# Performance work log

Hardware: AMD Instinct MI355X
Metric: run time of the kernel (lower is better)

The kernel has to match this reference:

```python
import jax, jax.numpy as jnp
import numpy as np

B, S, D, H = 2, 2048, 1024, 16
DK = D // H

def setup_inputs() -> dict:
    key = jax.random.key(0)
    ks = jax.random.split(key, 8)
    inp = {
        "Q": jax.random.normal(ks[0], (B, S, D), dtype=jnp.float32),
        "K": jax.random.normal(ks[1], (B, S, D), dtype=jnp.float32),
        "V": jax.random.normal(ks[2], (B, S, D), dtype=jnp.float32),
        "mask": jax.random.randint(ks[3], (B, 1, S, S), 0, 2, dtype=jnp.int32),
        # nn.Linear weights, shape [out_features, in_features], no bias
        "Wq": jax.random.normal(ks[4], (D, D), dtype=jnp.float32) / np.sqrt(D),
        "Wk": jax.random.normal(ks[5], (D, D), dtype=jnp.float32) / np.sqrt(D),
        "Wv": jax.random.normal(ks[6], (D, D), dtype=jnp.float32) / np.sqrt(D),
        "Wo": jax.random.normal(ks[7], (D, D), dtype=jnp.float32) / np.sqrt(D),
    }
    return inp

def reference(Q, K, V, mask, Wq, Wk, Wv, Wo):
    b, s, d = Q.shape
    # projections: y = x @ W.T (torch nn.Linear convention)
    q = (Q @ Wq.T).reshape(b, s, H, DK).transpose(0, 2, 1, 3)  # [b,h,s,dk]
    k = (K @ Wk.T).reshape(b, -1, H, DK).transpose(0, 2, 1, 3)
    v = (V @ Wv.T).reshape(b, -1, H, DK).transpose(0, 2, 1, 3)
    score = jnp.einsum("bhqd,bhkd->bhqk", q, k) / jnp.sqrt(jnp.float32(DK))
    # faithful to source: masked positions get value 1e-9 BEFORE softmax
    score = jnp.where(mask == 0, jnp.float32(1e-9), score)
    attn = jax.nn.softmax(score, axis=-1)
    # dropout p=0.1 treated as eval-mode identity
    out = jnp.einsum("bhqk,bhkd->bhqd", attn, v)  # [b,h,s,dk]
    out = out.transpose(0, 2, 1, 3).reshape(b, s, d)
    return out @ Wo.T
```

## Files before the change

### kernel.cpp

```cpp
#include <hip/hip_runtime.h>

typedef unsigned short u16;
typedef unsigned char  u8;
typedef unsigned long long u64;
typedef __attribute__((ext_vector_type(8))) short bf16x8;
typedef __attribute__((ext_vector_type(4))) float f32x4;

constexpr int B_  = 2;
constexpr int S_  = 2048;
constexpr int D_  = 1024;
constexpr int H_  = 16;
constexpr int DK_ = 64;
constexpr int NROW = B_ * S_;
constexpr size_t QSZ  = (size_t)B_ * H_ * S_ * DK_;
constexpr size_t XBSZ = (size_t)NROW * D_;
constexpr size_t WBSZ = (size_t)D_ * D_;
constexpr size_t MSZ  = (size_t)B_ * S_ * S_;
constexpr size_t MPKB = MSZ / 8;

__device__ __forceinline__ u16 f2bf(float f) {
    union { float f; unsigned u; } c; c.f = f;
    unsigned r = c.u + 0x7fffu + ((c.u >> 16) & 1u);
    return (u16)(r >> 16);
}
__device__ __forceinline__ unsigned pack2(float a, float b) {
    return (unsigned)f2bf(a) | ((unsigned)f2bf(b) << 16);
}
__device__ __forceinline__ unsigned cvt_pk_bf16(float a, float b) {
    unsigned r;
    asm("v_cvt_pk_bf16_f32 %0, %1, %2" : "=v"(r) : "v"(a), "v"(b));
    return r;
}

__device__ __forceinline__ void gl_lds16(const u16* g, u16* l) {
    __builtin_amdgcn_global_load_lds(
        (const __attribute__((address_space(1))) void*)g,
        (__attribute__((address_space(3))) void*)l, 16, 0, 0);
}

__global__ __launch_bounds__(256)
void cvt7m(const float* __restrict__ s0, const float* __restrict__ s1,
           const float* __restrict__ s2, const float* __restrict__ s3,
           const float* __restrict__ s4, const float* __restrict__ s5,
           const float* __restrict__ s6, const int* __restrict__ mk,
           u16* __restrict__ d0, u16* __restrict__ d1, u16* __restrict__ d2,
           u16* __restrict__ d3, u16* __restrict__ d4, u16* __restrict__ d5,
           u16* __restrict__ d6, u8* __restrict__ mp)
{
    constexpr size_t XT = 3 * XBSZ;
    constexpr int NCF = (int)((3 * XBSZ + 4 * WBSZ) / 2048);
    constexpr int NCM = (int)(MSZ / 2048);

    for (int c = blockIdx.x; c < NCF + NCM; c += gridDim.x) {
        if (c < NCF) {
            const size_t base = (size_t)c * 2048;
            const float* s; u16* d; size_t off;
            if (base < XT) {
                const int a = (int)(base >> 22);
                off = base & (XBSZ - 1);
                s = (a == 0) ? s0 : (a == 1) ? s1 : s2;
                d = (a == 0) ? d0 : (a == 1) ? d1 : d2;
            } else {
                const size_t r = base - XT;
                const int a = (int)(r >> 20);
                off = r & (WBSZ - 1);
                s = (a == 0) ? s3 : (a == 1) ? s4 : (a == 2) ? s5 : s6;
                d = (a == 0) ? d3 : (a == 1) ? d4 : (a == 2) ? d5 : d6;
            }
            const size_t e = off + (size_t)threadIdx.x * 8;
            const float4 x0 = *(const float4*)(s + e);
            const float4 x1 = *(const float4*)(s + e + 4);
            uint4 p;
            p.x = pack2(x0.x, x0.y); p.y = pack2(x0.z, x0.w);
            p.z = pack2(x1.x, x1.y); p.w = pack2(x1.z, x1.w);
            *(uint4*)(d + e) = p;
        } else {
            const size_t e = (size_t)(c - NCF) * 2048 + (size_t)threadIdx.x * 8;
            const int4 x0 = *(const int4*)(mk + e);
            const int4 x1 = *(const int4*)(mk + e + 4);
            unsigned bv = (unsigned)(x0.x != 0)        | ((unsigned)(x0.y != 0) << 1)
                        | ((unsigned)(x0.z != 0) << 2) | ((unsigned)(x0.w != 0) << 3)
                        | ((unsigned)(x1.x != 0) << 4) | ((unsigned)(x1.y != 0) << 5)
                        | ((unsigned)(x1.z != 0) << 6) | ((unsigned)(x1.w != 0) << 7);
            mp[e >> 3] = (u8)bv;
        }
    }
}

__global__ __launch_bounds__(256, 3)
void qkv_gemm(const u16* __restrict__ Xq, const u16* __restrict__ Xk,
              const u16* __restrict__ Xv,
              const u16* __restrict__ Wq, const u16* __restrict__ Wk,
              const u16* __restrict__ Wv,
              u16* __restrict__ Yq, u16* __restrict__ Yk, u16* __restrict__ Yv)
{
    __shared__ u16 As[128 * 32];
    __shared__ u16 Bs[128 * 32];

    const int z = blockIdx.z;
    const u16* X = (z == 0) ? Xq : (z == 1) ? Xk : Xv;
    const u16* W = (z == 0) ? Wq : (z == 1) ? Wk : Wv;
    u16*       Y = (z == 0) ? Yq : (z == 1) ? Yk : Yv;
    const float osc = (z == 0) ? 0.125f : 1.0f;

    const int tid  = threadIdx.x;
    const int lane = tid & 63;
    const int w    = tid >> 6;
    const int quad = lane >> 4;
    const int lq   = lane & 15;
    const int wm   = (w & 1) << 6;
    const int wn   = (w >> 1) << 6;

    const int m0 = blockIdx.x << 7;
    const int n0 = blockIdx.y << 7;

    const int srow = tid >> 2;
    const int scol = (tid & 3) << 3;
    const u16* ga0 = X + (size_t)(m0 + srow) * D_ + scol;
    const u16* ga1 = ga0 + (size_t)64 * D_;
    const u16* gb0 = W + (size_t)(n0 + srow) * D_ + scol;
    const u16* gb1 = gb0 + (size_t)64 * D_;

    u16* la0 = As + (size_t)w * 512;
    u16* la1 = As + 2048 + (size_t)w * 512;
    u16* lb0 = Bs + (size_t)w * 512;
    u16* lb1 = Bs + 2048 + (size_t)w * 512;

    f32x4 acc[4][4];
#pragma unroll
    for (int i = 0; i < 4; ++i)
#pragma unroll
        for (int j = 0; j < 4; ++j) acc[i][j] = (f32x4){0.f, 0.f, 0.f, 0.f};

    for (int kt = 0; kt < D_; kt += 32) {
        __syncthreads();
        gl_lds16(ga0 + kt, la0);
        gl_lds16(ga1 + kt, la1);
        gl_lds16(gb0 + kt, lb0);
        gl_lds16(gb1 + kt, lb1);
        __syncthreads();

        bf16x8 af[4], bf[4];
#pragma unroll
        for (int t = 0; t < 4; ++t) {
            af[t] = *(const bf16x8*)&As[(size_t)(wm + (t << 4) + lq) * 32 + (quad << 3)];
            bf[t] = *(const bf16x8*)&Bs[(size_t)(wn + (t << 4) + lq) * 32 + (quad << 3)];
        }
#pragma unroll
        for (int i = 0; i < 4; ++i)
#pragma unroll
            for (int j = 0; j < 4; ++j)
                acc[i][j] = __builtin_amdgcn_mfma_f32_16x16x32_bf16(
                    af[i], bf[j], acc[i][j], 0, 0, 0);
    }

#pragma unroll
    for (int i = 0; i < 4; ++i)
#pragma unroll
        for (int j = 0; j < 4; ++j)
#pragma unroll
            for (int r = 0; r < 4; ++r) {
                const int grow = m0 + wm + (i << 4) + (quad << 2) + r;
                const int of   = n0 + wn + (j << 4) + lq;
                const int b = grow >> 11, s = grow & (S_ - 1);
                const int h = of >> 6,    dk = of & 63;
                Y[(((size_t)(b * H_ + h)) * S_ + s) * DK_ + dk] =
                    f2bf(acc[i][j][r] * osc);
            }
}

__global__ __launch_bounds__(256, 3)
void out_gemm(const u16* __restrict__ X, const u16* __restrict__ W,
              float* __restrict__ Y)
{
    __shared__ u16 As[128 * 32];
    __shared__ u16 Bs[128 * 32];

    const int tid  = threadIdx.x;
    const int lane = tid & 63;
    const int w    = tid >> 6;
    const int quad = lane >> 4;
    const int lq   = lane & 15;
    const int wm   = (w & 1) << 6;
    const int wn   = (w >> 1) << 6;

    const int m0 = blockIdx.x << 7;
    const int n0 = blockIdx.y << 7;

    const int srow = tid >> 2;
    const int scol = (tid & 3) << 3;
    const u16* ga0 = X + (size_t)(m0 + srow) * D_ + scol;
    const u16* ga1 = ga0 + (size_t)64 * D_;
    const u16* gb0 = W + (size_t)(n0 + srow) * D_ + scol;
    const u16* gb1 = gb0 + (size_t)64 * D_;

    u16* la0 = As + (size_t)w * 512;
    u16* la1 = As + 2048 + (size_t)w * 512;
    u16* lb0 = Bs + (size_t)w * 512;
    u16* lb1 = Bs + 2048 + (size_t)w * 512;

    f32x4 acc[4][4];
#pragma unroll
    for (int i = 0; i < 4; ++i)
#pragma unroll
        for (int j = 0; j < 4; ++j) acc[i][j] = (f32x4){0.f, 0.f, 0.f, 0.f};

    for (int kt = 0; kt < D_; kt += 32) {
        __syncthreads();
        gl_lds16(ga0 + kt, la0);
        gl_lds16(ga1 + kt, la1);
        gl_lds16(gb0 + kt, lb0);
        gl_lds16(gb1 + kt, lb1);
        __syncthreads();

        bf16x8 af[4], bf[4];
#pragma unroll
        for (int t = 0; t < 4; ++t) {
            af[t] = *(const bf16x8*)&As[(size_t)(wm + (t << 4) + lq) * 32 + (quad << 3)];
            bf[t] = *(const bf16x8*)&Bs[(size_t)(wn + (t << 4) + lq) * 32 + (quad << 3)];
        }
#pragma unroll
        for (int i = 0; i < 4; ++i)
#pragma unroll
            for (int j = 0; j < 4; ++j)
                acc[i][j] = __builtin_amdgcn_mfma_f32_16x16x32_bf16(
                    af[i], bf[j], acc[i][j], 0, 0, 0);
    }

#pragma unroll
    for (int i = 0; i < 4; ++i)
#pragma unroll
        for (int j = 0; j < 4; ++j)
#pragma unroll
            for (int r = 0; r < 4; ++r) {
                const int grow = m0 + wm + (i << 4) + (quad << 2) + r;
                const int gcol = n0 + wn + (j << 4) + lq;
                Y[(size_t)grow * D_ + gcol] = acc[i][j][r];
            }
}

constexpr int AP = 72;

__global__ __launch_bounds__(256, 2)
void attn_mfma5(const u16* __restrict__ qb, const u16* __restrict__ kb,
                const u16* __restrict__ vb, const u8* __restrict__ mpk,
                u16* __restrict__ ctx)
{
    __shared__ u16 Qs[128][AP];
    __shared__ u16 Ks[64][AP];
    __shared__ u16 Vt[64][AP];
    __shared__ u16 Ps[128][AP];

    const int tid  = threadIdx.x;
    const int lane = tid & 63;
    const int w    = tid >> 6;
    const int quad = lane >> 4;
    const int lq   = lane & 15;
    const int w32  = w << 5;

    const int q0 = blockIdx.x << 7;
    const int h  = blockIdx.y;
    const int b  = blockIdx.z;

    const u16* qbh = qb + (((size_t)b * H_ + h) * S_ + q0) * DK_;
    const u16* kbh = kb + ((size_t)b * H_ + h) * S_ * DK_;
    const u16* vbh = vb + ((size_t)b * H_ + h) * S_ * DK_;
    const u8*  mbh = mpk + (size_t)b * S_ * (S_ / 8);

    {
        const int r = tid >> 1, c = (tid & 1) << 5;
#pragma unroll
        for (int u = 0; u < 4; ++u)
            *(uint4*)&Qs[r][c + (u << 3)] =
                *(const uint4*)&qbh[(size_t)r * DK_ + c + (u << 3)];
    }
    __syncthreads();
    bf16x8 aQ[2][2];
#pragma unroll
    for (int i = 0; i < 2; ++i) {
        aQ[i][0] = *(const bf16x8*)&Qs[w32 + (i << 4) + lq][quad << 3];
        aQ[i][1] = *(const bf16x8*)&Qs[w32 + (i << 4) + lq][32 + (quad << 3)];
    }

    f32x4 O[2][4];
    float lsum[2][4];
#pragma unroll
    for (int i = 0; i < 2; ++i)
#pragma unroll
        for (int t = 0; t < 4; ++t) O[i][t] = (f32x4){0.f, 0.f, 0.f, 0.f};
#pragma unroll
    for (int i = 0; i < 2; ++i)
#pragma unroll
        for (int r = 0; r < 4; ++r) lsum[i][r] = 0.f;

    const int ksr = tid >> 2, ksc = (tid & 3) << 4;
    const int vkey = lane, vsc = w << 4;
    const int vpc  = ((vkey & 15) << 2) | (vkey >> 4);

    uint4 kr0, kr1; ushort4 vr[4];
    {
        kr0 = *(const uint4*)&kbh[(size_t)ksr * DK_ + ksc];
        kr1 = *(const uint4*)&kbh[(size_t)ksr * DK_ + ksc + 8];
#pragma unroll
        for (int u = 0; u < 4; ++u)
            vr[u] = *(const ushort4*)&vbh[(size_t)vkey * DK_ + vsc + (u << 2)];
    }

    const int qrow0 = q0 + w32 + (quad << 2);
    const u8* mrow = mbh + (size_t)qrow0 * (S_ / 8);

    for (int k0 = 0; k0 < S_; k0 += 64) {
        u64 mw[2][4];
#pragma unroll
        for (int i = 0; i < 2; ++i)
#pragma unroll
            for (int r = 0; r < 4; ++r)
                mw[i][r] = *(const u64*)&mrow[(size_t)((i << 4) + r) * (S_ / 8) + (k0 >> 3)];

        __syncthreads();
        {
            *(uint4*)&Ks[ksr][ksc]     = kr0;
            *(uint4*)&Ks[ksr][ksc + 8] = kr1;
            const u16 vv[16] = {
                vr[0].x, vr[0].y, vr[0].z, vr[0].w,
                vr[1].x, vr[1].y, vr[1].z, vr[1].w,
                vr[2].x, vr[2].y, vr[2].z, vr[2].w,
                vr[3].x, vr[3].y, vr[3].z, vr[3].w };
#pragma unroll
            for (int i = 0; i < 16; ++i)
                Vt[vsc + i][vpc] = vv[i];
        }
        __syncthreads();

        if (k0 + 64 < S_) {
            const size_t kb0 = (size_t)(k0 + 64 + ksr) * DK_ + ksc;
            kr0 = *(const uint4*)&kbh[kb0];
            kr1 = *(const uint4*)&kbh[kb0 + 8];
            const size_t vb0 = (size_t)(k0 + 64 + vkey) * DK_ + vsc;
#pragma unroll
            for (int u = 0; u < 4; ++u)
                vr[u] = *(const ushort4*)&vbh[vb0 + (u << 2)];
        }

        f32x4 st[2][4];
#pragma unroll
        for (int t = 0; t < 4; ++t) {
            const bf16x8 b0 = *(const bf16x8*)&Ks[(t << 4) + lq][quad << 3];
            const bf16x8 b1 = *(const bf16x8*)&Ks[(t << 4) + lq][32 + (quad << 3)];
#pragma unroll
            for (int i = 0; i < 2; ++i) {
                f32x4 c = {0.f, 0.f, 0.f, 0.f};
                c = __builtin_amdgcn_mfma_f32_16x16x32_bf16(aQ[i][0], b0, c, 0, 0, 0);
                c = __builtin_amdgcn_mfma_f32_16x16x32_bf16(aQ[i][1], b1, c, 0, 0, 0);
                st[i][t] = c;
            }
        }

#pragma unroll
        for (int i = 0; i < 2; ++i)
#pragma unroll
            for (int r = 0; r < 4; ++r) {
                const unsigned lo = (unsigned)mw[i][r];
                const unsigned hi = (unsigned)(mw[i][r] >> 32);
                float p0 = __expf(st[i][0][r]);
                float p1 = __expf(st[i][1][r]);
                float p2 = __expf(st[i][2][r]);
                float p3 = __expf(st[i][3][r]);
                p0 = ((lo >> lq) & 1u) ? p0 : 1.0f;
                p1 = ((lo >> (lq + 16)) & 1u) ? p1 : 1.0f;
                p2 = ((hi >> lq) & 1u) ? p2 : 1.0f;
                p3 = ((hi >> (lq + 16)) & 1u) ? p3 : 1.0f;
                lsum[i][r] += (p0 + p1) + (p2 + p3);
                uint2 pw;
                pw.x = cvt_pk_bf16(p0, p1);
                pw.y = cvt_pk_bf16(p2, p3);
                *(uint2*)&Ps[w32 + (i << 4) + (quad << 2) + r][lq << 2] = pw;
            }

        bf16x8 aP[2][2];
#pragma unroll
        for (int i = 0; i < 2; ++i) {
            aP[i][0] = *(const bf16x8*)&Ps[w32 + (i << 4) + lq][quad << 3];
            aP[i][1] = *(const bf16x8*)&Ps[w32 + (i << 4) + lq][32 + (quad << 3)];
        }
#pragma unroll
        for (int t = 0; t < 4; ++t) {
            const bf16x8 b0 = *(const bf16x8*)&Vt[(t << 4) + lq][quad << 3];
            const bf16x8 b1 = *(const bf16x8*)&Vt[(t << 4) + lq][32 + (quad << 3)];
#pragma unroll
            for (int i = 0; i < 2; ++i) {
                O[i][t] = __builtin_amdgcn_mfma_f32_16x16x32_bf16(aP[i][0], b0, O[i][t], 0, 0, 0);
                O[i][t] = __builtin_amdgcn_mfma_f32_16x16x32_bf16(aP[i][1], b1, O[i][t], 0, 0, 0);
            }
        }
    }

#pragma unroll
    for (int i = 0; i < 2; ++i)
#pragma unroll
        for (int r = 0; r < 4; ++r) {
#pragma unroll
            for (int off = 1; off < 16; off <<= 1)
                lsum[i][r] += __shfl_xor(lsum[i][r], off);
            lsum[i][r] = 1.0f / lsum[i][r];
        }

#pragma unroll
    for (int i = 0; i < 2; ++i)
#pragma unroll
        for (int t = 0; t < 4; ++t)
#pragma unroll
            for (int r = 0; r < 4; ++r) {
                const int row = qrow0 + (i << 4) + r;
                ctx[((size_t)b * S_ + row) * D_ + (h << 6) + (t << 4) + lq] =
                    f2bf(O[i][t][r] * lsum[i][r]);
            }
}

extern "C" void kernel_launch(void* const* d_in, const int* in_sizes, int n_in,
                              void* d_out, int out_size, void* d_ws, size_t ws_size,
                              hipStream_t stream)
{
    const float* Q    = (const float*)d_in[0];
    const float* K    = (const float*)d_in[1];
    const float* V    = (const float*)d_in[2];
    const int*   mask = (const int*)d_in[3];
    const float* Wq   = (const float*)d_in[4];
    const float* Wk   = (const float*)d_in[5];
    const float* Wv   = (const float*)d_in[6];
    const float* Wo   = (const float*)d_in[7];
    float* out = (float*)d_out;

    u16* xqb = (u16*)d_ws;
    u16* xkb = xqb + XBSZ;
    u16* xvb = xqb + 2 * XBSZ;
    u16* wqb = xqb + 3 * XBSZ;
    u16* wkb = wqb + WBSZ;
    u16* wvb = wqb + 2 * WBSZ;
    u16* wob = wqb + 3 * WBSZ;
    u16* qw  = wqb + 4 * WBSZ;
    u16* kw  = qw + QSZ;
    u16* vw  = qw + 2 * QSZ;
    u8*  mpk = (u8*)(qw + 3 * QSZ);
    u16* cx  = xqb;

    const dim3 blk(256);

    hipLaunchKernelGGL(cvt7m, dim3(2048), blk, 0, stream,
                       Q, K, V, Wq, Wk, Wv, Wo, mask,
                       xqb, xkb, xvb, wqb, wkb, wvb, wob, mpk);
    hipLaunchKernelGGL(qkv_gemm, dim3(NROW / 128, D_ / 128, 3), blk, 0, stream,
                       xqb, xkb, xvb, wqb, wkb, wvb, qw, kw, vw);
    hipLaunchKernelGGL(attn_mfma5, dim3(S_ / 128, H_, B_), blk, 0, stream,
                       qw, kw, vw, mpk, cx);
    hipLaunchKernelGGL(out_gemm, dim3(NROW / 128, D_ / 128), blk, 0, stream,
                       cx, wob, out);
}
```

Before: 254.8 us.

## Split attention key range across two warp groups and merge partial results

```diff
diff --git a/kernel.cpp b/kernel.cpp
--- a/kernel.cpp
+++ b/kernel.cpp
@@ -222,7 +222,7 @@
 #pragma unroll
         for (int i = 0; i < 4; ++i)
 #pragma unroll
-            for (int j = 0; j < 4; ++j)
+            for (int j = 0; j < 2 * 2; ++j)
                 acc[i][j] = __builtin_amdgcn_mfma_f32_16x16x32_bf16(
                     af[i], bf[j], acc[i][j], 0, 0, 0);
     }
@@ -241,45 +241,39 @@
 
 constexpr int AP = 72;
 
-__global__ __launch_bounds__(256, 2)
-void attn_mfma5(const u16* __restrict__ qb, const u16* __restrict__ kb,
+__global__ __launch_bounds__(512, 4)
+void attn_mfma6(const u16* __restrict__ qb, const u16* __restrict__ kb,
                 const u16* __restrict__ vb, const u8* __restrict__ mpk,
                 u16* __restrict__ ctx)
 {
-    __shared__ u16 Qs[128][AP];
-    __shared__ u16 Ks[64][AP];
-    __shared__ u16 Vt[64][AP];
-    __shared__ u16 Ps[128][AP];
+    __shared__ __align__(16) u16 Ks[2][64][AP];
+    __shared__ __align__(16) u16 Vt[2][64][AP];
+    __shared__ __align__(16) u16 Ps[2][128][AP];
 
     const int tid  = threadIdx.x;
     const int lane = tid & 63;
     const int w    = tid >> 6;
+    const int g    = w >> 2;
+    const int wl   = w & 3;
     const int quad = lane >> 4;
     const int lq   = lane & 15;
-    const int w32  = w << 5;
+    const int w32  = wl << 5;
+    const int tg   = tid & 255;
 
     const int q0 = blockIdx.x << 7;
     const int h  = blockIdx.y;
     const int b  = blockIdx.z;
 
     const u16* qbh = qb + (((size_t)b * H_ + h) * S_ + q0) * DK_;
-    const u16* kbh = kb + ((size_t)b * H_ + h) * S_ * DK_;
-    const u16* vbh = vb + ((size_t)b * H_ + h) * S_ * DK_;
-    const u8*  mbh = mpk + (size_t)b * S_ * (S_ / 8);
-
-    {
-        const int r = tid >> 1, c = (tid & 1) << 5;
-#pragma unroll
-        for (int u = 0; u < 4; ++u)
-            *(uint4*)&Qs[r][c + (u << 3)] =
-                *(const uint4*)&qbh[(size_t)r * DK_ + c + (u << 3)];
-    }
-    __syncthreads();
+    const u16* kbh = kb + ((size_t)b * H_ + h) * S_ * DK_ + ((size_t)(g << 10)) * DK_;
+    const u16* vbh = vb + ((size_t)b * H_ + h) * S_ * DK_ + ((size_t)(g << 10)) * DK_;
+
     bf16x8 aQ[2][2];
 #pragma unroll
     for (int i = 0; i < 2; ++i) {
-        aQ[i][0] = *(const bf16x8*)&Qs[w32 + (i << 4) + lq][quad << 3];
-        aQ[i][1] = *(const bf16x8*)&Qs[w32 + (i << 4) + lq][32 + (quad << 3)];
+        const size_t qr = (size_t)(w32 + (i << 4) + lq) * DK_;
+        aQ[i][0] = *(const bf16x8*)&qbh[qr + (quad << 3)];
+        aQ[i][1] = *(const bf16x8*)&qbh[qr + 32 + (quad << 3)];
     }
 
     f32x4 O[2][4];
@@ -293,8 +287,8 @@
 #pragma unroll
         for (int r = 0; r < 4; ++r) lsum[i][r] = 0.f;
 
-    const int ksr = tid >> 2, ksc = (tid & 3) << 4;
-    const int vkey = lane, vsc = w << 4;
+    const int ksr = tg >> 2, ksc = (tg & 3) << 4;
+    const int vkey = tg & 63, vsc = (tg >> 6) << 4;
     const int vpc  = ((vkey & 15) << 2) | (vkey >> 4);
 
     uint4 kr0, kr1; ushort4 vr[4];
@@ -307,20 +301,21 @@
     }
 
     const int qrow0 = q0 + w32 + (quad << 2);
-    const u8* mrow = mbh + (size_t)qrow0 * (S_ / 8);
-
-    for (int k0 = 0; k0 < S_; k0 += 64) {
+    const u8* mrow = mpk + (size_t)b * S_ * (S_ / 8)
+                   + (size_t)qrow0 * (S_ / 8) + (g << 7);
+
+    for (int kk = 0; kk < 1024; kk += 64) {
         u64 mw[2][4];
 #pragma unroll
         for (int i = 0; i < 2; ++i)
 #pragma unroll
             for (int r = 0; r < 4; ++r)
-                mw[i][r] = *(const u64*)&mrow[(size_t)((i << 4) + r) * (S_ / 8) + (k0 >> 3)];
+                mw[i][r] = *(const u64*)&mrow[(size_t)((i << 4) + r) * (S_ / 8) + (kk >> 3)];
 
         __syncthreads();
         {
-            *(uint4*)&Ks[ksr][ksc]     = kr0;
-            *(uint4*)&Ks[ksr][ksc + 8] = kr1;
+            *(uint4*)&Ks[g][ksr][ksc]     = kr0;
+            *(uint4*)&Ks[g][ksr][ksc + 8] = kr1;
             const u16 vv[16] = {
                 vr[0].x, vr[0].y, vr[0].z, vr[0].w,
                 vr[1].x, vr[1].y, vr[1].z, vr[1].w,
@@ -328,15 +323,15 @@
                 vr[3].x, vr[3].y, vr[3].z, vr[3].w };
 #pragma unroll
             for (int i = 0; i < 16; ++i)
-                Vt[vsc + i][vpc] = vv[i];
-        }
-        __syncthreads();
-
-        if (k0 + 64 < S_) {
-            const size_t kb0 = (size_t)(k0 + 64 + ksr) * DK_ + ksc;
+                Vt[g][vsc + i][vpc] = vv[i];
+        }
+        __syncthreads();
+
+        if (kk + 64 < 1024) {
+            const size_t kb0 = (size_t)(kk + 64 + ksr) * DK_ + ksc;
             kr0 = *(const uint4*)&kbh[kb0];
             kr1 = *(const uint4*)&kbh[kb0 + 8];
-            const size_t vb0 = (size_t)(k0 + 64 + vkey) * DK_ + vsc;
+            const size_t vb0 = (size_t)(kk + 64 + vkey) * DK_ + vsc;
 #pragma unroll
             for (int u = 0; u < 4; ++u)
                 vr[u] = *(const ushort4*)&vbh[vb0 + (u << 2)];
@@ -345,8 +340,8 @@
         f32x4 st[2][4];
 #pragma unroll
         for (int t = 0; t < 4; ++t) {
-            const bf16x8 b0 = *(const bf16x8*)&Ks[(t << 4) + lq][quad << 3];
-            const bf16x8 b1 = *(const bf16x8*)&Ks[(t << 4) + lq][32 + (quad << 3)];
+            const bf16x8 b0 = *(const bf16x8*)&Ks[g][(t << 4) + lq][quad << 3];
+            const bf16x8 b1 = *(const bf16x8*)&Ks[g][(t << 4) + lq][32 + (quad << 3)];
 #pragma unroll
             for (int i = 0; i < 2; ++i) {
                 f32x4 c = {0.f, 0.f, 0.f, 0.f};
@@ -374,19 +369,19 @@
                 uint2 pw;
                 pw.x = cvt_pk_bf16(p0, p1);
                 pw.y = cvt_pk_bf16(p2, p3);
-                *(uint2*)&Ps[w32 + (i << 4) + (quad << 2) + r][lq << 2] = pw;
+                *(uint2*)&Ps[g][w32 + (i << 4) + (quad << 2) + r][lq << 2] = pw;
             }
 
         bf16x8 aP[2][2];
 #pragma unroll
         for (int i = 0; i < 2; ++i) {
-            aP[i][0] = *(const bf16x8*)&Ps[w32 + (i << 4) + lq][quad << 3];
-            aP[i][1] = *(const bf16x8*)&Ps[w32 + (i << 4) + lq][32 + (quad << 3)];
+            aP[i][0] = *(const bf16x8*)&Ps[g][w32 + (i << 4) + lq][quad << 3];
+            aP[i][1] = *(const bf16x8*)&Ps[g][w32 + (i << 4) + lq][32 + (quad << 3)];
         }
 #pragma unroll
         for (int t = 0; t < 4; ++t) {
-            const bf16x8 b0 = *(const bf16x8*)&Vt[(t << 4) + lq][quad << 3];
-            const bf16x8 b1 = *(const bf16x8*)&Vt[(t << 4) + lq][32 + (quad << 3)];
+            const bf16x8 b0 = *(const bf16x8*)&Vt[g][(t << 4) + lq][quad << 3];
+            const bf16x8 b1 = *(const bf16x8*)&Vt[g][(t << 4) + lq][32 + (quad << 3)];
 #pragma unroll
             for (int i = 0; i < 2; ++i) {
                 O[i][t] = __builtin_amdgcn_mfma_f32_16x16x32_bf16(aP[i][0], b0, O[i][t], 0, 0, 0);
@@ -394,6 +389,40 @@
             }
         }
     }
+
+    __syncthreads();
+    float* cbO = (float*)&Ps[0][0][0];
+    float* cbL = (float*)&Ks[0][0][0];
+    if (g == 1) {
+        const int t1 = tid - 256;
+#pragma unroll
+        for (int i = 0; i < 2; ++i)
+#pragma unroll
+            for (int t = 0; t < 4; ++t)
+#pragma unroll
+                for (int r = 0; r < 4; ++r)
+                    cbO[t1 * 33 + (i << 4) + (t << 2) + r] = O[i][t][r];
+#pragma unroll
+        for (int i = 0; i < 2; ++i)
+#pragma unroll
+            for (int r = 0; r < 4; ++r)
+                cbL[t1 * 9 + (i << 2) + r] = lsum[i][r];
+    }
+    __syncthreads();
+    if (g == 1) return;
+
+#pragma unroll
+    for (int i = 0; i < 2; ++i)
+#pragma unroll
+        for (int t = 0; t < 4; ++t)
+#pragma unroll
+            for (int r = 0; r < 4; ++r)
+                O[i][t][r] += cbO[tid * 33 + (i << 4) + (t << 2) + r];
+#pragma unroll
+    for (int i = 0; i < 2; ++i)
+#pragma unroll
+        for (int r = 0; r < 4; ++r)
+            lsum[i][r] += cbL[tid * 9 + (i << 2) + r];
 
 #pragma unroll
     for (int i = 0; i < 2; ++i)
@@ -444,15 +473,13 @@
     u8*  mpk = (u8*)(qw + 3 * QSZ);
     u16* cx  = xqb;
 
-    const dim3 blk(256);
-
-    hipLaunchKernelGGL(cvt7m, dim3(2048), blk, 0, stream,
+    hipLaunchKernelGGL(cvt7m, dim3(2048), dim3(256), 0, stream,
                        Q, K, V, Wq, Wk, Wv, Wo, mask,
                        xqb, xkb, xvb, wqb, wkb, wvb, wob, mpk);
-    hipLaunchKernelGGL(qkv_gemm, dim3(NROW / 128, D_ / 128, 3), blk, 0, stream,
+    hipLaunchKernelGGL(qkv_gemm, dim3(NROW / 128, D_ / 128, 3), dim3(256), 0, stream,
                        xqb, xkb, xvb, wqb, wkb, wvb, qw, kw, vw);
-    hipLaunchKernelGGL(attn_mfma5, dim3(S_ / 128, H_, B_), blk, 0, stream,
+    hipLaunchKernelGGL(attn_mfma6, dim3(S_ / 128, H_, B_), dim3(512), 0, stream,
                        qw, kw, vw, mpk, cx);
-    hipLaunchKernelGGL(out_gemm, dim3(NROW / 128, D_ / 128), blk, 0, stream,
+    hipLaunchKernelGGL(out_gemm, dim3(NROW / 128, D_ / 128), dim3(256), 0, stream,
                        cx, wob, out);
 }
```

Result: slower. 294.1 us (+15.4%).

## Halve attention query tile to 64 rows and swizzle block-to-head mapping

Applied to the files above, without the earlier changes.

```diff
diff --git a/kernel.cpp b/kernel.cpp
--- a/kernel.cpp
+++ b/kernel.cpp
@@ -241,57 +241,48 @@
 
 constexpr int AP = 72;
 
-__global__ __launch_bounds__(256, 2)
-void attn_mfma5(const u16* __restrict__ qb, const u16* __restrict__ kb,
+__global__ __launch_bounds__(256, 4)
+void attn_mfma7(const u16* __restrict__ qb, const u16* __restrict__ kb,
                 const u16* __restrict__ vb, const u8* __restrict__ mpk,
                 u16* __restrict__ ctx)
 {
-    __shared__ u16 Qs[128][AP];
-    __shared__ u16 Ks[64][AP];
-    __shared__ u16 Vt[64][AP];
-    __shared__ u16 Ps[128][AP];
+    __shared__ __align__(16) u16 Ks[64][AP];
+    __shared__ __align__(16) u16 Vt[64][AP];
+    __shared__ __align__(16) u16 Ps[64][AP];
 
     const int tid  = threadIdx.x;
     const int lane = tid & 63;
     const int w    = tid >> 6;
     const int quad = lane >> 4;
     const int lq   = lane & 15;
-    const int w32  = w << 5;
-
-    const int q0 = blockIdx.x << 7;
-    const int h  = blockIdx.y;
-    const int b  = blockIdx.z;
+    const int w16  = w << 4;
+
+    const int bid = blockIdx.x + (int)(gridDim.x * (blockIdx.y + gridDim.y * blockIdx.z));
+    const int nwg = (int)(gridDim.x * gridDim.y * gridDim.z);
+    const int swz = (bid & 7) * (nwg >> 3) + (bid >> 3);
+    const int qt = swz & 31;
+    const int h  = (swz >> 5) & 15;
+    const int b  = swz >> 9;
+
+    const int q0 = qt << 6;
 
     const u16* qbh = qb + (((size_t)b * H_ + h) * S_ + q0) * DK_;
     const u16* kbh = kb + ((size_t)b * H_ + h) * S_ * DK_;
     const u16* vbh = vb + ((size_t)b * H_ + h) * S_ * DK_;
-    const u8*  mbh = mpk + (size_t)b * S_ * (S_ / 8);
-
+
+    bf16x8 aQ0, aQ1;
     {
-        const int r = tid >> 1, c = (tid & 1) << 5;
-#pragma unroll
-        for (int u = 0; u < 4; ++u)
-            *(uint4*)&Qs[r][c + (u << 3)] =
-                *(const uint4*)&qbh[(size_t)r * DK_ + c + (u << 3)];
-    }
-    __syncthreads();
-    bf16x8 aQ[2][2];
-#pragma unroll
-    for (int i = 0; i < 2; ++i) {
-        aQ[i][0] = *(const bf16x8*)&Qs[w32 + (i << 4) + lq][quad << 3];
-        aQ[i][1] = *(const bf16x8*)&Qs[w32 + (i << 4) + lq][32 + (quad << 3)];
-    }
-
-    f32x4 O[2][4];
-    float lsum[2][4];
-#pragma unroll
-    for (int i = 0; i < 2; ++i)
-#pragma unroll
-        for (int t = 0; t < 4; ++t) O[i][t] = (f32x4){0.f, 0.f, 0.f, 0.f};
-#pragma unroll
-    for (int i = 0; i < 2; ++i)
-#pragma unroll
-        for (int r = 0; r < 4; ++r) lsum[i][r] = 0.f;
+        const size_t qr = (size_t)(w16 + lq) * DK_;
+        aQ0 = *(const bf16x8*)&qbh[qr + (quad << 3)];
+        aQ1 = *(const bf16x8*)&qbh[qr + 32 + (quad << 3)];
+    }
+
+    f32x4 O[4];
+    float lsum[4];
+#pragma unroll
+    for (int t = 0; t < 4; ++t) O[t] = (f32x4){0.f, 0.f, 0.f, 0.f};
+#pragma unroll
+    for (int r = 0; r < 4; ++r) lsum[r] = 0.f;
 
     const int ksr = tid >> 2, ksc = (tid & 3) << 4;
     const int vkey = lane, vsc = w << 4;
@@ -306,16 +297,14 @@
             vr[u] = *(const ushort4*)&vbh[(size_t)vkey * DK_ + vsc + (u << 2)];
     }
 
-    const int qrow0 = q0 + w32 + (quad << 2);
-    const u8* mrow = mbh + (size_t)qrow0 * (S_ / 8);
+    const int qrow0 = q0 + w16 + (quad << 2);
+    const u8* mrow = mpk + (size_t)b * S_ * (S_ / 8) + (size_t)qrow0 * (S_ / 8);
 
     for (int k0 = 0; k0 < S_; k0 += 64) {
-        u64 mw[2][4];
-#pragma unroll
-        for (int i = 0; i < 2; ++i)
-#pragma unroll
-            for (int r = 0; r < 4; ++r)
-                mw[i][r] = *(const u64*)&mrow[(size_t)((i << 4) + r) * (S_ / 8) + (k0 >> 3)];
+        u64 mw[4];
+#pragma unroll
+        for (int r = 0; r < 4; ++r)
+            mw[r] = *(const u64*)&mrow[(size_t)r * (S_ / 8) + (k0 >> 3)];
 
         __syncthreads();
         {
@@ -342,79 +331,64 @@
                 vr[u] = *(const ushort4*)&vbh[vb0 + (u << 2)];
         }
 
-        f32x4 st[2][4];
+        f32x4 st[4];
 #pragma unroll
         for (int t = 0; t < 4; ++t) {
             const bf16x8 b0 = *(const bf16x8*)&Ks[(t << 4) + lq][quad << 3];
             const bf16x8 b1 = *(const bf16x8*)&Ks[(t << 4) + lq][32 + (quad << 3)];
-#pragma unroll
-            for (int i = 0; i < 2; ++i) {
-                f32x4 c = {0.f, 0.f, 0.f, 0.f};
-                c = __builtin_amdgcn_mfma_f32_16x16x32_bf16(aQ[i][0], b0, c, 0, 0, 0);
-                c = __builtin_amdgcn_mfma_f32_16x16x32_bf16(aQ[i][1], b1, c, 0, 0, 0);
-                st[i][t] = c;
-            }
-        }
-
-#pragma unroll
-        for (int i = 0; i < 2; ++i)
-#pragma unroll
-            for (int r = 0; r < 4; ++r) {
-                const unsigned lo = (unsigned)mw[i][r];
-                const unsigned hi = (unsigned)(mw[i][r] >> 32);
-                float p0 = __expf(st[i][0][r]);
-                float p1 = __expf(st[i][1][r]);
-                float p2 = __expf(st[i][2][r]);
-                float p3 = __expf(st[i][3][r]);
-                p0 = ((lo >> lq) & 1u) ? p0 : 1.0f;
-                p1 = ((lo >> (lq + 16)) & 1u) ? p1 : 1.0f;
-                p2 = ((hi >> lq) & 1u) ? p2 : 1.0f;
-                p3 = ((hi >> (lq + 16)) & 1u) ? p3 : 1.0f;
-                lsum[i][r] += (p0 + p1) + (p2 + p3);
-                uint2 pw;
-                pw.x = cvt_pk_bf16(p0, p1);
-                pw.y = cvt_pk_bf16(p2, p3);
-                *(uint2*)&Ps[w32 + (i << 4) + (quad << 2) + r][lq << 2] = pw;
-            }
-
-        bf16x8 aP[2][2];
-#pragma unroll
-        for (int i = 0; i < 2; ++i) {
-            aP[i][0] = *(const bf16x8*)&Ps[w32 + (i << 4) + lq][quad << 3];
-            aP[i][1] = *(const bf16x8*)&Ps[w32 + (i << 4) + lq][32 + (quad << 3)];
-        }
+            f32x4 c = {0.f, 0.f, 0.f, 0.f};
+            c = __builtin_amdgcn_mfma_f32_16x16x32_bf16(aQ0, b0, c, 0, 0, 0);
+            c = __builtin_amdgcn_mfma_f32_16x16x32_bf16(aQ1, b1, c, 0, 0, 0);
+            st[t] = c;
+        }
+
+#pragma unroll
+        for (int r = 0; r < 4; ++r) {
+            const unsigned lo = (unsigned)mw[r];
+            const unsigned hi = (unsigned)(mw[r] >> 32);
+            float p0 = __expf(st[0][r]);
+            float p1 = __expf(st[1][r]);
+            float p2 = __expf(st[2][r]);
+            float p3 = __expf(st[3][r]);
+            p0 = ((lo >> lq) & 1u) ? p0 : 1.0f;
+            p1 = ((lo >> (lq + 16)) & 1u) ? p1 : 1.0f;
+            p2 = ((hi >> lq) & 1u) ? p2 : 1.0f;
+            p3 = ((hi >> (lq + 16)) & 1u) ? p3 : 1.0f;
+            lsum[r] += (p0 + p1) + (p2 + p3);
+            uint2 pw;
+            pw.x = cvt_pk_bf16(p0, p1);
+            pw.y = cvt_pk_bf16(p2, p3);
+            *(uint2*)&Ps[w16 + (quad << 2) + r][lq << 2] = pw;
+        }
+
+        bf16x8 aP0, aP1;
+        aP0 = *(const bf16x8*)&Ps[w16 + lq][quad << 3];
+        aP1 = *(const bf16x8*)&Ps[w16 + lq][32 + (quad << 3)];
 #pragma unroll
         for (int t = 0; t < 4; ++t) {
             const bf16x8 b0 = *(const bf16x8*)&Vt[(t << 4) + lq][quad << 3];
             const bf16x8 b1 = *(const bf16x8*)&Vt[(t << 4) + lq][32 + (quad << 3)];
-#pragma unroll
-            for (int i = 0; i < 2; ++i) {
-                O[i][t] = __builtin_amdgcn_mfma_f32_16x16x32_bf16(aP[i][0], b0, O[i][t], 0, 0, 0);
-                O[i][t] = __builtin_amdgcn_mfma_f32_16x16x32_bf16(aP[i][1], b1, O[i][t], 0, 0, 0);
-            }
-        }
-    }
-
-#pragma unroll
-    for (int i = 0; i < 2; ++i)
+            O[t] = __builtin_amdgcn_mfma_f32_16x16x32_bf16(aP0, b0, O[t], 0, 0, 0);
+            O[t] = __builtin_amdgcn_mfma_f32_16x16x32_bf16(aP1, b1, O[t], 0, 0, 0);
+        }
+    }
+
+#pragma unroll
+    for (int r = 0; r < 4; ++r) {
+#pragma unroll
+        for (int off = 1; off < 16; off <<= 1)
+            lsum[r] += __shfl_xor(lsum[r], off);
+        lsum[r] = 1.0f / lsum[r];
+    }
+
+#pragma unroll
+    for (int t = 0; t < 4; ++t)
 #pragma unroll
         for (int r = 0; r < 4; ++r) {
-#pragma unroll
-            for (int off = 1; off < 16; off <<= 1)
-                lsum[i][r] += __shfl_xor(lsum[i][r], off);
-            lsum[i][r] = 1.0f / lsum[i][r];
-        }
-
-#pragma unroll
-    for (int i = 0; i < 2; ++i)
-#pragma unroll
-        for (int t = 0; t < 4; ++t)
-#pragma unroll
-            for (int r = 0; r < 4; ++r) {
-                const int row = qrow0 + (i << 4) + r;
-                ctx[((size_t)b * S_ + row) * D_ + (h << 6) + (t << 4) + lq] =
-                    f2bf(O[i][t][r] * lsum[i][r]);
-            }
+            const int row = qrow0 + r;
+            ctx[((size_t)b * S_ + row) * D_ + (h << 6) + (t << 4) + lq] =
+                f2bf(O[t][r] * lsum[r]);
+        }
 }
 
 extern "C" void kernel_launch(void* const* d_in, const int* in_sizes, int n_in,
@@ -444,15 +418,13 @@
     u8*  mpk = (u8*)(qw + 3 * QSZ);
     u16* cx  = xqb;
 
-    const dim3 blk(256);
-
-    hipLaunchKernelGGL(cvt7m, dim3(2048), blk, 0, stream,
+    hipLaunchKernelGGL(cvt7m, dim3(2048), dim3(256), 0, stream,
                        Q, K, V, Wq, Wk, Wv, Wo, mask,
                        xqb, xkb, xvb, wqb, wkb, wvb, wob, mpk);
-    hipLaunchKernelGGL(qkv_gemm, dim3(NROW / 128, D_ / 128, 3), blk, 0, stream,
+    hipLaunchKernelGGL(qkv_gemm, dim3(NROW / 128, D_ / 128, 3), dim3(256), 0, stream,
                        xqb, xkb, xvb, wqb, wkb, wvb, qw, kw, vw);
-    hipLaunchKernelGGL(attn_mfma5, dim3(S_ / 128, H_, B_), blk, 0, stream,
+    hipLaunchKernelGGL(attn_mfma7, dim3(S_ / 64, H_, B_), dim3(256), 0, stream,
                        qw, kw, vw, mpk, cx);
-    hipLaunchKernelGGL(out_gemm, dim3(NROW / 128, D_ / 128), blk, 0, stream,
+    hipLaunchKernelGGL(out_gemm, dim3(NROW / 128, D_ / 128), dim3(256), 0, stream,
                        cx, wob, out);
 }
```

Measured after the change: 264.1 us. +3.6%, slower.
